# Optimization experiments

Hardware: AMD Instinct MI355X
Metric: run time of the kernel (lower is better)

## Reference

```python
import jax, jax.numpy as jnp
import numpy as np

B, C, H, W = 4, 256, 64, 64
N = H * W


def _conv1x1(x, w, b):
    # x: [B,C,H,W], w: [O,C], b: [O]  (1x1 conv == per-pixel linear)
    return jnp.einsum('bchw,oc->bohw', x, w) + b[None, :, None, None]


def setup_inputs() -> dict:
    key = jax.random.key(0)
    ks = jax.random.split(key, 11)
    s = 1.0 / np.sqrt(C)
    x = jax.random.normal(ks[0], (B, C, H, W), dtype=jnp.float32)
    mkw = lambda k: jax.random.normal(k, (C, C), dtype=jnp.float32) * s
    mkb = lambda k: jax.random.normal(k, (C,), dtype=jnp.float32) * 0.01
    return {
        'x': x,
        'w_teta': mkw(ks[1]), 'b_teta': mkb(ks[2]),
        'w_fi': mkw(ks[3]), 'b_fi': mkb(ks[4]),
        'w_gi': mkw(ks[5]), 'b_gi': mkb(ks[6]),
        'w_o1': mkw(ks[7]), 'b_o1': mkb(ks[8]),
        'w_o2': mkw(ks[9]), 'b_o2': mkb(ks[10]),
    }


def reference(x, w_teta, b_teta, w_fi, b_fi, w_gi, b_gi, w_o1, b_o1, w_o2, b_o2):
    b, c, h, w = x.shape
    n = h * w
    # 1x1 projections, flattened to [B,C,N]
    x1 = _conv1x1(x, w_teta, b_teta).reshape(b, c, n)
    x2 = _conv1x1(x, w_fi, b_fi).reshape(b, c, n)
    x3 = _conv1x1(x, w_gi, b_gi).reshape(b, c, n)
    # NOTE: original uses .view (memory reinterpretation), NOT transpose
    x1 = x1.reshape(b, n, c)
    x3 = x3.reshape(b, n, c)
    scores = jnp.einsum('bnc,bcm->bnm', x1, x2)      # [B,N,N]
    s_row = jax.nn.softmax(scores, axis=2)
    s_col = jax.nn.softmax(scores, axis=1)
    y1 = jnp.einsum('bnm,bmc->bnc', s_row, x3)       # [B,N,C]
    y2 = jnp.einsum('bnm,bmc->bnc', s_col, x3)
    # transpose(1,2) then view -> contiguous transpose + reshape
    y1 = jnp.swapaxes(y1, 1, 2).reshape(b, c, h, w)
    y2 = jnp.swapaxes(y2, 1, 2).reshape(b, c, h, w)
    o1 = _conv1x1(y1, w_o1, b_o1)
    o2 = _conv1x1(y2, w_o2, b_o2)
    xx = jnp.concatenate([x, x], axis=1)             # [B,2C,H,W]
    agg = jnp.concatenate([o1, o2], axis=1)
    return jax.nn.relu(xx + agg)
```

## Files before the change

kernel.cpp:

```cpp
#include <hip/hip_runtime.h>

#define BB   4
#define CC   256
#define NPIX 4096
#define AST2 40
#define YST  72

typedef __attribute__((ext_vector_type(8)))  short bf16x8;
typedef __attribute__((ext_vector_type(8)))  _Float16 f16x8;
typedef __attribute__((ext_vector_type(4)))  short short4v;
typedef __attribute__((ext_vector_type(16))) float f32x16;

__device__ __forceinline__ short f2h(float f) {
    _Float16 h = (_Float16)f;
    return __builtin_bit_cast(short, h);
}
__device__ __forceinline__ int cdrow(int r, int l5) {
    return (r & 3) + 8 * (r >> 2) + 4 * l5;
}
__device__ __forceinline__ short s_enc(float v) {
    float c = fmaxf(fminf(v, 127.9f), -127.9f);
    return (short)__float2int_rn(c * 256.0f);
}
__device__ __forceinline__ float s_dec(short v) {
    return (float)v * (1.0f / 256.0f);
}

__device__ __forceinline__ void mfma_core_f16(
    const short* __restrict__ A, const short* __restrict__ B, f32x16 acc[2][2])
{
    __shared__ short LA[128 * AST2], LB[128 * AST2];
    const int t = threadIdx.x;
    const int lane = t & 63, w = t >> 6;
    const int l31 = lane & 31, l5 = lane >> 5;
    const int nq = (w & 1) * 64, mq = (w >> 1) * 64;
    const int sr = t >> 1;
    const int sk = (t & 1) * 16;
    const size_t gs = (size_t)sr * 256 + sk;
    const int ls = sr * AST2 + sk;

    bf16x8 rA0 = *(const bf16x8*)(A + gs);
    bf16x8 rA1 = *(const bf16x8*)(A + gs + 8);
    bf16x8 rB0 = *(const bf16x8*)(B + gs);
    bf16x8 rB1 = *(const bf16x8*)(B + gs + 8);

    for (int k0 = 0; k0 < 256; k0 += 32) {
        __syncthreads();
        *(bf16x8*)&LA[ls]     = rA0;
        *(bf16x8*)&LA[ls + 8] = rA1;
        *(bf16x8*)&LB[ls]     = rB0;
        *(bf16x8*)&LB[ls + 8] = rB1;
        __syncthreads();
        if (k0 + 32 < 256) {
            size_t g = gs + k0 + 32;
            rA0 = *(const bf16x8*)(A + g);
            rA1 = *(const bf16x8*)(A + g + 8);
            rB0 = *(const bf16x8*)(B + g);
            rB1 = *(const bf16x8*)(B + g + 8);
        }
#pragma unroll
        for (int ks = 0; ks < 2; ks++) {
            f16x8 a[2], b[2];
#pragma unroll
            for (int s = 0; s < 2; s++) {
                a[s] = *(const f16x8*)&LA[(nq + s * 32 + l31) * AST2 + ks * 16 + l5 * 8];
                b[s] = *(const f16x8*)&LB[(mq + s * 32 + l31) * AST2 + ks * 16 + l5 * 8];
            }
#pragma unroll
            for (int s = 0; s < 2; s++)
#pragma unroll
                for (int u = 0; u < 2; u++)
                    acc[s][u] = __builtin_amdgcn_mfma_f32_32x32x16_f16(a[s], b[u], acc[s][u], 0, 0, 0);
        }
    }
}


__global__ __launch_bounds__(256) void pack_w5(
    const float* __restrict__ w0, const float* __restrict__ w1,
    const float* __restrict__ w2, const float* __restrict__ w3,
    const float* __restrict__ w4, short* __restrict__ wall)
{
    int which = blockIdx.y;
    const float* w = which == 0 ? w0 : which == 1 ? w1 : which == 2 ? w2
                   : which == 3 ? w3 : w4;
    int idx = blockIdx.x * 1024 + threadIdx.x * 4;
    float4 v = *(const float4*)(w + idx);
    short4v h;
    h.x = f2h(v.x); h.y = f2h(v.y); h.z = f2h(v.z); h.w = f2h(v.w);
    *(short4v*)(wall + which * 65536 + idx) = h;
}

__global__ __launch_bounds__(256) void pack_t_f16(
    const float* __restrict__ in, short* __restrict__ o16)
{
    __shared__ short T[32][36];
    const int b  = blockIdx.z;
    const int n0 = blockIdx.x * 32;
    const int c0 = blockIdx.y * 32;
    const float* src = in + (size_t)b * CC * NPIX;
    const int t = threadIdx.x;
    const int r = t >> 3, q = t & 7;
    float4 v = *(const float4*)(src + (size_t)(c0 + r) * NPIX + n0 + q * 4);
    T[q * 4 + 0][r] = f2h(v.x);
    T[q * 4 + 1][r] = f2h(v.y);
    T[q * 4 + 2][r] = f2h(v.z);
    T[q * 4 + 3][r] = f2h(v.w);
    __syncthreads();
    short4v o;
    o.x = T[r][q * 4 + 0];
    o.y = T[r][q * 4 + 1];
    o.z = T[r][q * 4 + 2];
    o.w = T[r][q * 4 + 3];
    size_t oo = (size_t)b * CC * NPIX + (size_t)(n0 + r) * 256 + c0 + q * 4;
    *(short4v*)(o16 + oo) = o;
}

__global__ __launch_bounds__(256) void tr16_cn(
    const short* __restrict__ in, short* __restrict__ outp)
{
    __shared__ short T[32][33];
    const int b  = blockIdx.z;
    const int n0 = blockIdx.x * 32;
    const int c0 = blockIdx.y * 32;
    const short* src = in + (size_t)b * CC * NPIX;
    short* dst = outp + (size_t)b * CC * NPIX;
    const int t = threadIdx.x;
    const int r = t >> 3, q = t & 7;
    short4v v = *(const short4v*)(src + (size_t)(c0 + r) * NPIX + n0 + q * 4);
    T[q * 4 + 0][r] = v.x;
    T[q * 4 + 1][r] = v.y;
    T[q * 4 + 2][r] = v.z;
    T[q * 4 + 3][r] = v.w;
    __syncthreads();
    short4v o;
    o.x = T[r][q * 4 + 0];
    o.y = T[r][q * 4 + 1];
    o.z = T[r][q * 4 + 2];
    o.w = T[r][q * 4 + 3];
    *(short4v*)(dst + (size_t)(n0 + r) * 256 + c0 + q * 4) = o;
}

__global__ __launch_bounds__(256) void packVt_bf(
    const short* __restrict__ x3f, short* __restrict__ Vt)
{
    __shared__ short T[32][33];
    const int b  = blockIdx.z;
    const int m0 = blockIdx.x * 32;
    const int c0 = blockIdx.y * 32;
    const short* in = x3f + (size_t)b * CC * NPIX;
    short* out = Vt + (size_t)b * CC * NPIX;
    const int t = threadIdx.x;
    const int r = t >> 3, q = t & 7;
    short4v v = *(const short4v*)(in + (size_t)(m0 + r) * CC + c0 + q * 4);
    T[q * 4 + 0][r] = v.x;
    T[q * 4 + 1][r] = v.y;
    T[q * 4 + 2][r] = v.z;
    T[q * 4 + 3][r] = v.w;
    __syncthreads();
    short4v o;
    o.x = T[r][q * 4 + 0];
    o.y = T[r][q * 4 + 1];
    o.z = T[r][q * 4 + 2];
    o.w = T[r][q * 4 + 3];
    *(short4v*)(out + (size_t)(c0 + r) * NPIX + m0 + q * 4) = o;
}


__global__ __launch_bounds__(256) void proj_mfma(
    const short* __restrict__ wpf, const short* __restrict__ xtf,
    const float* __restrict__ b_teta, const float* __restrict__ b_fi,
    const float* __restrict__ b_gi,
    short* __restrict__ x1f, short* __restrict__ x2f, short* __restrict__ x3f)
{
    const int z = blockIdx.z, p = z >> 2, b = z & 3;
    const int n0 = blockIdx.x * 128, c0 = blockIdx.y * 128;
    const size_t CN = (size_t)CC * NPIX;
    const short* Ah = wpf + p * 65536 + c0 * 256;
    const short* Bh = xtf + (size_t)b * CN + (size_t)n0 * 256;
    const float* bias = p == 0 ? b_teta : p == 1 ? b_fi : b_gi;
    short* dst = p == 0 ? x1f : p == 1 ? x2f : x3f;

    f32x16 acc[2][2] = {};
    mfma_core_f16(Ah, Bh, acc);

    const int t = threadIdx.x, lane = t & 63, w = t >> 6;
    const int l31 = lane & 31, l5 = lane >> 5;
    const int aq = (w & 1) * 64, bq = (w >> 1) * 64;
#pragma unroll
    for (int s = 0; s < 2; s++)
#pragma unroll
        for (int u = 0; u < 2; u++)
#pragma unroll
            for (int r = 0; r < 16; r++) {
                int c = c0 + aq + s * 32 + cdrow(r, l5);
                int n = n0 + bq + u * 32 + l31;
                float v = acc[s][u][r] + bias[c];
                size_t o = (size_t)b * CN + (size_t)c * NPIX + n;
                dst[o] = f2h(v);
            }
}

__global__ __launch_bounds__(256, 2) void scores_mfma(
    const short* __restrict__ x1f, const short* __restrict__ x2tf,
    short* __restrict__ S16, float* __restrict__ pm, float* __restrict__ pl)
{
    __shared__ short LA[256 * AST2];
    __shared__ short LB[128 * AST2];
    const int m0 = blockIdx.x * 128, n0 = blockIdx.y * 256;
    const short* A = x1f + (size_t)n0 * 256;
    const short* B = x2tf + (size_t)m0 * 256;

    const int t = threadIdx.x, lane = t & 63, w = t >> 6;
    const int l31 = lane & 31, l5 = lane >> 5;
    const int h = w & 1, g = w >> 1;

    const size_t gsA = (size_t)t * 256;
    const int lsA = t * AST2;
    const int srB = t >> 1, skB = (t & 1) * 16;
    const size_t gsB = (size_t)srB * 256 + skB;
    const int lsB = srB * AST2 + skB;

    bf16x8 rA0 = *(const bf16x8*)(A + gsA);
    bf16x8 rA1 = *(const bf16x8*)(A + gsA + 8);
    bf16x8 rA2 = *(const bf16x8*)(A + gsA + 16);
    bf16x8 rA3 = *(const bf16x8*)(A + gsA + 24);
    bf16x8 rB0 = *(const bf16x8*)(B + gsB);
    bf16x8 rB1 = *(const bf16x8*)(B + gsB + 8);

    f32x16 acc[4][2] = {};

    for (int k0 = 0; k0 < 256; k0 += 32) {
        __syncthreads();
        *(bf16x8*)&LA[lsA]      = rA0;
        *(bf16x8*)&LA[lsA + 8]  = rA1;
        *(bf16x8*)&LA[lsA + 16] = rA2;
        *(bf16x8*)&LA[lsA + 24] = rA3;
        *(bf16x8*)&LB[lsB]      = rB0;
        *(bf16x8*)&LB[lsB + 8]  = rB1;
        __syncthreads();
        if (k0 + 32 < 256) {
            size_t gA = gsA + k0 + 32;
            size_t gB = gsB + k0 + 32;
            rA0 = *(const bf16x8*)(A + gA);
            rA1 = *(const bf16x8*)(A + gA + 8);
            rA2 = *(const bf16x8*)(A + gA + 16);
            rA3 = *(const bf16x8*)(A + gA + 24);
            rB0 = *(const bf16x8*)(B + gB);
            rB1 = *(const bf16x8*)(B + gB + 8);
        }
#pragma unroll
        for (int ks = 0; ks < 2; ks++) {
            f16x8 a[4], b[2];
#pragma unroll
            for (int s = 0; s < 4; s++)
                a[s] = *(const f16x8*)&LA[(h * 128 + s * 32 + l31) * AST2 + ks * 16 + l5 * 8];
#pragma unroll
            for (int u = 0; u < 2; u++)
                b[u] = *(const f16x8*)&LB[(g * 64 + u * 32 + l31) * AST2 + ks * 16 + l5 * 8];
#pragma unroll
            for (int s = 0; s < 4; s++)
#pragma unroll
                for (int u = 0; u < 2; u++)
                    acc[s][u] = __builtin_amdgcn_mfma_f32_32x32x16_f16(a[s], b[u], acc[s][u], 0, 0, 0);
        }
    }

#pragma unroll
    for (int s = 0; s < 4; s++)
#pragma unroll
        for (int u = 0; u < 2; u++)
#pragma unroll
            for (int r = 0; r < 16; r++) {
                int n = n0 + h * 128 + s * 32 + cdrow(r, l5);
                int m = m0 + g * 64 + u * 32 + l31;
                S16[(size_t)n * NPIX + m] = s_enc(acc[s][u][r]);
            }

#pragma unroll
    for (int u = 0; u < 2; u++) {
        float vmax = -1e30f;
#pragma unroll
        for (int s = 0; s < 4; s++)
#pragma unroll
            for (int r = 0; r < 16; r++) vmax = fmaxf(vmax, acc[s][u][r]);
        float vsum = 0.0f;
#pragma unroll
        for (int s = 0; s < 4; s++)
#pragma unroll
            for (int r = 0; r < 16; r++) vsum += __expf(acc[s][u][r] - vmax);
        float vmax2 = __shfl_xor(vmax, 32, 64);
        float vsum2 = __shfl_xor(vsum, 32, 64);
        float mc = fmaxf(vmax, vmax2);
        float sc = vsum * __expf(vmax - mc) + vsum2 * __expf(vmax2 - mc);
        if (l5 == 0) {
            size_t pidx = (size_t)(blockIdx.y * 2 + h) * NPIX + m0 + g * 64 + u * 32 + l31;
            pm[pidx] = mc;
            pl[pidx] = sc;
        }
    }
}

__global__ __launch_bounds__(256) void out_mfma(
    const short* __restrict__ wof,
    const float* __restrict__ b_o1, const float* __restrict__ b_o2,
    const short* __restrict__ Yp,
    const float* __restrict__ x, float* __restrict__ out, int b)
{
    __shared__ short LA[128 * AST2], LB[128 * AST2];
    const size_t CN_ = (size_t)NPIX * CC;
    const int ch0 = blockIdx.y * 128;
    const int pix0 = blockIdx.x * 128;
    const int mode = ch0 < 256 ? 0 : 1;
    const short* W = wof + mode * 65536 + (size_t)(ch0 & 255) * 256;
    const short* Yq = Yp + (size_t)mode * 4 * CN_;
    const float* bias = mode == 0 ? b_o1 : b_o2;

    const int t = threadIdx.x, lane = t & 63, w = t >> 6;
    const int l31 = lane & 31, l5 = lane >> 5;
    const int nq = (w & 1) * 64, mq = (w >> 1) * 64;
    const int sr = t >> 1;
    const int sk = (t & 1) * 16;
    const size_t gsA = (size_t)sr * 256 + sk;
    const size_t gsB = (size_t)(pix0 + sr) * 256 + sk;
    const int ls = sr * AST2 + sk;

    f32x16 acc[2][2] = {};

    bf16x8 rA0 = *(const bf16x8*)(W + gsA);
    bf16x8 rA1 = *(const bf16x8*)(W + gsA + 8);
    f16x8 rB0, rB1;
    {
        rB0 = *(const f16x8*)(Yq + gsB);
        rB1 = *(const f16x8*)(Yq + gsB + 8);
#pragma unroll
        for (int q = 1; q < 4; q++) {
            rB0 = rB0 + *(const f16x8*)(Yq + (size_t)q * CN_ + gsB);
            rB1 = rB1 + *(const f16x8*)(Yq + (size_t)q * CN_ + gsB + 8);
        }
    }

    for (int k0 = 0; k0 < 256; k0 += 32) {
        __syncthreads();
        *(bf16x8*)&LA[ls]    = rA0;
        *(bf16x8*)&LA[ls + 8] = rA1;
        *(f16x8*)&LB[ls]     = rB0;
        *(f16x8*)&LB[ls + 8] = rB1;
        __syncthreads();
        if (k0 + 32 < 256) {
            size_t gA = gsA + k0 + 32;
            size_t gB = gsB + k0 + 32;
            rA0 = *(const bf16x8*)(W + gA);
            rA1 = *(const bf16x8*)(W + gA + 8);
            rB0 = *(const f16x8*)(Yq + gB);
            rB1 = *(const f16x8*)(Yq + gB + 8);
#pragma unroll
            for (int q = 1; q < 4; q++) {
                rB0 = rB0 + *(const f16x8*)(Yq + (size_t)q * CN_ + gB);
                rB1 = rB1 + *(const f16x8*)(Yq + (size_t)q * CN_ + gB + 8);
            }
        }
#pragma unroll
        for (int ks = 0; ks < 2; ks++) {
            f16x8 a[2], bb[2];
#pragma unroll
            for (int s = 0; s < 2; s++) {
                a[s]  = *(const f16x8*)&LA[(nq + s * 32 + l31) * AST2 + ks * 16 + l5 * 8];
                bb[s] = *(const f16x8*)&LB[(mq + s * 32 + l31) * AST2 + ks * 16 + l5 * 8];
            }
#pragma unroll
            for (int s = 0; s < 2; s++)
#pragma unroll
                for (int u = 0; u < 2; u++)
                    acc[s][u] = __builtin_amdgcn_mfma_f32_32x32x16_f16(a[s], bb[u], acc[s][u], 0, 0, 0);
        }
    }

    const int aq = (w & 1) * 64, bq = (w >> 1) * 64;
#pragma unroll
    for (int s = 0; s < 2; s++)
#pragma unroll
        for (int u = 0; u < 2; u++)
#pragma unroll
            for (int r = 0; r < 16; r++) {
                int ch = ch0 + aq + s * 32 + cdrow(r, l5);
                int pix = pix0 + bq + u * 32 + l31;
                int chm = ch & 255;
                float v = acc[s][u][r] + bias[chm] +
                          x[((size_t)b * CC + chm) * NPIX + pix];
                out[((size_t)b * 2 * CC + ch) * NPIX + pix] = fmaxf(v, 0.0f);
            }
}

__global__ __launch_bounds__(256) void stats16_kernel(
    const short* __restrict__ S16,
    const float* __restrict__ pm, const float* __restrict__ pl,
    float* __restrict__ cm, float* __restrict__ cli,
    float* __restrict__ rm, float* __restrict__ rli)
{
    __shared__ float sm[4][64], sl[4][64];
    __shared__ float red[4];
    const int t = threadIdx.x;
    if (blockIdx.x < 64) {
        const int cl = t & 63, ch = t >> 6;
        const int col = blockIdx.x * 64 + cl;
        float m = -1e30f, l = 0.0f;
        for (int i = ch * 8; i < ch * 8 + 8; i++) {
            float m2 = pm[(size_t)i * NPIX + col];
            float l2 = pl[(size_t)i * NPIX + col];
            float mn = fmaxf(m, m2);
            l = l * __expf(m - mn) + l2 * __expf(m2 - mn);
            m = mn;
        }
        sm[ch][cl] = m;
        sl[ch][cl] = l;
        __syncthreads();
        if (ch == 0) {
#pragma unroll
            for (int j = 1; j < 4; j++) {
                float m2 = sm[j][cl], l2 = sl[j][cl];
                float mn = fmaxf(m, m2);
                l = l * __expf(m - mn) + l2 * __expf(m2 - mn);
                m = mn;
            }
            cm[col]  = m;
            cli[col] = 1.0f / l;
        }
    } else {
        const int row = blockIdx.x - 64;
        const short* sp = S16 + (size_t)row * NPIX;
        const int w = t >> 6, lane = t & 63;
        float s4[16];
#pragma unroll
        for (int i = 0; i < 4; i++) {
            short4v v = *(const short4v*)(sp + (i * 256 + t) * 4);
            s4[i * 4 + 0] = s_dec(v.x);
            s4[i * 4 + 1] = s_dec(v.y);
            s4[i * 4 + 2] = s_dec(v.z);
            s4[i * 4 + 3] = s_dec(v.w);
        }
        float m = -1e30f;
#pragma unroll
        for (int i = 0; i < 16; i++) m = fmaxf(m, s4[i]);
        for (int off = 32; off; off >>= 1) m = fmaxf(m, __shfl_xor(m, off, 64));
        if (lane == 0) red[w] = m;
        __syncthreads();
        m = fmaxf(fmaxf(red[0], red[1]), fmaxf(red[2], red[3]));
        __syncthreads();
        float sum = 0.0f;
#pragma unroll
        for (int i = 0; i < 16; i++) sum += __expf(s4[i] - m);
        for (int off = 32; off; off >>= 1) sum += __shfl_xor(sum, off, 64);
        if (lane == 0) red[w] = sum;
        __syncthreads();
        if (t == 0) {
            rm[row]  = m;
            rli[row] = 1.0f / (red[0] + red[1] + red[2] + red[3]);
        }
    }
}

__device__ __forceinline__ void compute_ph(
    const short4v sv[4], int mode, int mg,
    const float* __restrict__ cmv, const float* __restrict__ cliv,
    float mrow, float lrow, short4v ph[4])
{
    if (mode == 0) {
#pragma unroll
        for (int i = 0; i < 4; i++) {
            ph[i].x = f2h(__expf(s_dec(sv[i].x) - mrow) * lrow);
            ph[i].y = f2h(__expf(s_dec(sv[i].y) - mrow) * lrow);
            ph[i].z = f2h(__expf(s_dec(sv[i].z) - mrow) * lrow);
            ph[i].w = f2h(__expf(s_dec(sv[i].w) - mrow) * lrow);
        }
    } else {
#pragma unroll
        for (int i = 0; i < 4; i++) {
            float4 cm4 = *(const float4*)(cmv + mg + i * 4);
            float4 cl4 = *(const float4*)(cliv + mg + i * 4);
            ph[i].x = f2h(__expf(s_dec(sv[i].x) - cm4.x) * cl4.x);
            ph[i].y = f2h(__expf(s_dec(sv[i].y) - cm4.y) * cl4.y);
            ph[i].z = f2h(__expf(s_dec(sv[i].z) - cm4.z) * cl4.z);
            ph[i].w = f2h(__expf(s_dec(sv[i].w) - cm4.w) * cl4.w);
        }
    }
}

__global__ __launch_bounds__(256) void pv_kernel(
    const short* __restrict__ S16, const short* __restrict__ Vt,
    const float* __restrict__ rmv, const float* __restrict__ rliv,
    const float* __restrict__ cmv, const float* __restrict__ cliv,
    short* __restrict__ Yp)
{
    __shared__ short LA[64 * YST];
    __shared__ short LB[256 * YST];
    const int mode = blockIdx.z, kq = blockIdx.y;
    const int n0 = blockIdx.x * 64;
    const int kbase = kq * 1024;

    const int t = threadIdx.x, lane = t & 63, w = t >> 6;
    const int l31 = lane & 31, l5 = lane >> 5;
    const int nst = (w & 1) * 32, cb = (w >> 1) * 128;
    const int ar = t >> 2;
    const int ak = (t & 3) * 16;

    const float mrow = rmv[n0 + ar];
    const float lrow = rliv[n0 + ar];
    const short* sp = S16 + (size_t)(n0 + ar) * NPIX + kbase + ak;

    short4v svA[4], svB[4];
    bf16x8 pbA[8], pbB[8];
#pragma unroll
    for (int i = 0; i < 4; i++) {
        svA[i] = *(const short4v*)(sp + i * 4);
        svB[i] = *(const short4v*)(sp + 64 + i * 4);
    }
#pragma unroll
    for (int i = 0; i < 4; i++) {
        const short* bp0 = Vt + (size_t)(i * 64 + ar) * NPIX + kbase + ak;
        pbA[2 * i]     = *(const bf16x8*)bp0;
        pbA[2 * i + 1] = *(const bf16x8*)(bp0 + 8);
        pbB[2 * i]     = *(const bf16x8*)(bp0 + 64);
        pbB[2 * i + 1] = *(const bf16x8*)(bp0 + 72);
    }

    f32x16 acc[4] = {};
    for (int sx = 0; sx < 8; sx++) {
        const int s = sx * 2;
        {
            short4v ph[4];
            compute_ph(svA, mode, kbase + s * 64 + ak, cmv, cliv, mrow, lrow, ph);
            __syncthreads();
#pragma unroll
            for (int i = 0; i < 4; i++)
                *(short4v*)&LA[ar * YST + ak + i * 4] = ph[i];
#pragma unroll
            for (int i = 0; i < 4; i++) {
                *(bf16x8*)&LB[(i * 64 + ar) * YST + ak]     = pbA[2 * i];
                *(bf16x8*)&LB[(i * 64 + ar) * YST + ak + 8] = pbA[2 * i + 1];
            }
            __syncthreads();
            if (s + 2 < 16) {
                const short* spn = sp + (s + 2) * 64;
#pragma unroll
                for (int i = 0; i < 4; i++)
                    svA[i] = *(const short4v*)(spn + i * 4);
                int kg = kbase + (s + 2) * 64 + ak;
#pragma unroll
                for (int i = 0; i < 4; i++) {
                    const short* bp = Vt + (size_t)(i * 64 + ar) * NPIX + kg;
                    pbA[2 * i]     = *(const bf16x8*)bp;
                    pbA[2 * i + 1] = *(const bf16x8*)(bp + 8);
                }
            }
#pragma unroll
            for (int kc = 0; kc < 4; kc++) {
                f16x8 af = *(const f16x8*)&LA[(nst + l31) * YST + kc * 16 + l5 * 8];
#pragma unroll
                for (int u = 0; u < 4; u++) {
                    f16x8 bf = *(const f16x8*)&LB[(cb + u * 32 + l31) * YST + kc * 16 + l5 * 8];
                    acc[u] = __builtin_amdgcn_mfma_f32_32x32x16_f16(af, bf, acc[u], 0, 0, 0);
                }
            }
        }
        {
            short4v ph[4];
            compute_ph(svB, mode, kbase + (s + 1) * 64 + ak, cmv, cliv, mrow, lrow, ph);
            __syncthreads();
#pragma unroll
            for (int i = 0; i < 4; i++)
                *(short4v*)&LA[ar * YST + ak + i * 4] = ph[i];
#pragma unroll
            for (int i = 0; i < 4; i++) {
                *(bf16x8*)&LB[(i * 64 + ar) * YST + ak]     = pbB[2 * i];
                *(bf16x8*)&LB[(i * 64 + ar) * YST + ak + 8] = pbB[2 * i + 1];
            }
            __syncthreads();
            if (s + 3 < 16) {
                const short* spn = sp + (s + 3) * 64;
#pragma unroll
                for (int i = 0; i < 4; i++)
                    svB[i] = *(const short4v*)(spn + i * 4);
                int kg = kbase + (s + 3) * 64 + ak;
#pragma unroll
                for (int i = 0; i < 4; i++) {
                    const short* bp = Vt + (size_t)(i * 64 + ar) * NPIX + kg;
                    pbB[2 * i]     = *(const bf16x8*)bp;
                    pbB[2 * i + 1] = *(const bf16x8*)(bp + 8);
                }
            }
#pragma unroll
            for (int kc = 0; kc < 4; kc++) {
                f16x8 af = *(const f16x8*)&LA[(nst + l31) * YST + kc * 16 + l5 * 8];
#pragma unroll
                for (int u = 0; u < 4; u++) {
                    f16x8 bf = *(const f16x8*)&LB[(cb + u * 32 + l31) * YST + kc * 16 + l5 * 8];
                    acc[u] = __builtin_amdgcn_mfma_f32_32x32x16_f16(af, bf, acc[u], 0, 0, 0);
                }
            }
        }
    }

    short* Yo = Yp + (size_t)(mode * 4 + kq) * ((size_t)NPIX * CC);
#pragma unroll
    for (int u = 0; u < 4; u++)
#pragma unroll
        for (int r = 0; r < 16; r++) {
            int rr = cdrow(r, l5);
            Yo[(size_t)(n0 + nst + rr) * CC + cb + u * 32 + l31] = f2h(acc[u][r]);
        }
}

extern "C" void kernel_launch(void* const* d_in, const int* in_sizes, int n_in,
                              void* d_out, int out_size, void* d_ws, size_t ws_size,
                              hipStream_t stream)
{
    (void)in_sizes; (void)n_in; (void)out_size; (void)ws_size;
    const float* x      = (const float*)d_in[0];
    const float* w_teta = (const float*)d_in[1];
    const float* b_teta = (const float*)d_in[2];
    const float* w_fi   = (const float*)d_in[3];
    const float* b_fi   = (const float*)d_in[4];
    const float* w_gi   = (const float*)d_in[5];
    const float* b_gi   = (const float*)d_in[6];
    const float* w_o1   = (const float*)d_in[7];
    const float* b_o1   = (const float*)d_in[8];
    const float* w_o2   = (const float*)d_in[9];
    const float* b_o2   = (const float*)d_in[10];
    float* out = (float*)d_out;

    const size_t CN = (size_t)CC * NPIX;
    const size_t NN = (size_t)NPIX * NPIX;
    short* wsp   = (short*)d_ws;
    short* S16   = wsp;
    short* Yp    = S16 + NN;
    short* x1f   = Yp + 16 * CN;
    short* x2tf  = x1f + BB * CN;
    short* Vtb   = x2tf + BB * CN;
    float* cm    = (float*)(Vtb + BB * CN);
    float* cli   = cm + NPIX;
    float* rm    = cli + NPIX;
    float* rli   = rm + NPIX;
    float* pm    = rli + NPIX;
    float* pl    = pm + 64 * NPIX;
    short* wall  = (short*)(pl + 64 * NPIX);
    short* wpf   = wall;
    short* wof   = wall + 3 * 65536;
    short* xtf  = Yp;
    short* x2f  = S16;
    short* x3f  = S16 + BB * CN;

    dim3 blk(256);
    pack_w5<<<dim3(64, 5), blk, 0, stream>>>(w_teta, w_fi, w_gi, w_o1, w_o2, wall);
    pack_t_f16<<<dim3(128, 8, 4), blk, 0, stream>>>(x, xtf);

    proj_mfma<<<dim3(32, 2, 12), blk, 0, stream>>>(
        wpf, xtf, b_teta, b_fi, b_gi, x1f, x2f, x3f);

    tr16_cn<<<dim3(128, 8, 4), blk, 0, stream>>>(x2f, x2tf);
    packVt_bf<<<dim3(128, 8, 4), blk, 0, stream>>>(x3f, Vtb);

    for (int b = 0; b < BB; b++) {
        scores_mfma<<<dim3(32, 16), blk, 0, stream>>>(
            x1f + b * CN, x2tf + b * CN, S16, pm, pl);
        stats16_kernel<<<dim3(64 + NPIX), blk, 0, stream>>>(
            S16, pm, pl, cm, cli, rm, rli);
        pv_kernel<<<dim3(64, 4, 2), blk, 0, stream>>>(
            S16, Vtb + b * CN, rm, rli, cm, cli, Yp);
        out_mfma<<<dim3(32, 4), blk, 0, stream>>>(
            wof, b_o1, b_o2, Yp, x, out, b);
    }
}
```

Measured before the change: 448.9 us.

## Enlarge PV tile to 128 rows and split K into eight partial sums

The PV kernel now computes 128 query rows per block instead of 64, with each wave doing a 2x4 MFMA tile. The block covers 512 keys instead of 1024, so the K dimension is split into eight partial outputs. This raises reuse of the V tile staged in shared memory and simplifies the single-buffered loop. In exchange the output projection kernel must read and sum eight partial Y buffers instead of four, and the partial workspace doubles.

```diff
diff --git a/kernel.cpp b/kernel.cpp
--- a/kernel.cpp
+++ b/kernel.cpp
@@ -313,7 +313,7 @@
     const int pix0 = blockIdx.x * 128;
     const int mode = ch0 < 256 ? 0 : 1;
     const short* W = wof + mode * 65536 + (size_t)(ch0 & 255) * 256;
-    const short* Yq = Yp + (size_t)mode * 4 * CN_;
+    const short* Yq = Yp + (size_t)mode * 8 * CN_;
     const float* bias = mode == 0 ? b_o1 : b_o2;
 
     const int t = threadIdx.x, lane = t & 63, w = t >> 6;
@@ -334,7 +334,7 @@
         rB0 = *(const f16x8*)(Yq + gsB);
         rB1 = *(const f16x8*)(Yq + gsB + 8);
 #pragma unroll
-        for (int q = 1; q < 4; q++) {
+        for (int q = 1; q < 8; q++) {
             rB0 = rB0 + *(const f16x8*)(Yq + (size_t)q * CN_ + gsB);
             rB1 = rB1 + *(const f16x8*)(Yq + (size_t)q * CN_ + gsB + 8);
         }
@@ -355,7 +355,7 @@
             rB0 = *(const f16x8*)(Yq + gB);
             rB1 = *(const f16x8*)(Yq + gB + 8);
 #pragma unroll
-            for (int q = 1; q < 4; q++) {
+            for (int q = 1; q < 8; q++) {
                 rB0 = rB0 + *(const f16x8*)(Yq + (size_t)q * CN_ + gB);
                 rB1 = rB1 + *(const f16x8*)(Yq + (size_t)q * CN_ + gB + 8);
             }
@@ -460,155 +460,127 @@
     }
 }
 
-__device__ __forceinline__ void compute_ph(
-    const short4v sv[4], int mode, int mg,
-    const float* __restrict__ cmv, const float* __restrict__ cliv,
-    float mrow, float lrow, short4v ph[4])
-{
-    if (mode == 0) {
-#pragma unroll
-        for (int i = 0; i < 4; i++) {
-            ph[i].x = f2h(__expf(s_dec(sv[i].x) - mrow) * lrow);
-            ph[i].y = f2h(__expf(s_dec(sv[i].y) - mrow) * lrow);
-            ph[i].z = f2h(__expf(s_dec(sv[i].z) - mrow) * lrow);
-            ph[i].w = f2h(__expf(s_dec(sv[i].w) - mrow) * lrow);
-        }
-    } else {
-#pragma unroll
-        for (int i = 0; i < 4; i++) {
-            float4 cm4 = *(const float4*)(cmv + mg + i * 4);
-            float4 cl4 = *(const float4*)(cliv + mg + i * 4);
-            ph[i].x = f2h(__expf(s_dec(sv[i].x) - cm4.x) * cl4.x);
-            ph[i].y = f2h(__expf(s_dec(sv[i].y) - cm4.y) * cl4.y);
-            ph[i].z = f2h(__expf(s_dec(sv[i].z) - cm4.z) * cl4.z);
-            ph[i].w = f2h(__expf(s_dec(sv[i].w) - cm4.w) * cl4.w);
-        }
-    }
-}
-
 __global__ __launch_bounds__(256) void pv_kernel(
     const short* __restrict__ S16, const short* __restrict__ Vt,
     const float* __restrict__ rmv, const float* __restrict__ rliv,
     const float* __restrict__ cmv, const float* __restrict__ cliv,
     short* __restrict__ Yp)
 {
-    __shared__ short LA[64 * YST];
+    __shared__ short LA[128 * YST];
     __shared__ short LB[256 * YST];
     const int mode = blockIdx.z, kq = blockIdx.y;
-    const int n0 = blockIdx.x * 64;
-    const int kbase = kq * 1024;
+    const int n0 = blockIdx.x * 128;
+    const int kbase = kq * 512;
 
     const int t = threadIdx.x, lane = t & 63, w = t >> 6;
     const int l31 = lane & 31, l5 = lane >> 5;
-    const int nst = (w & 1) * 32, cb = (w >> 1) * 128;
-    const int ar = t >> 2;
-    const int ak = (t & 3) * 16;
+    const int nst = (w & 1) * 64, cb = (w >> 1) * 128;
+    const int ar = t >> 1;
+    const int ak = (t & 1) * 32;
+    const int br = t >> 1;
+    const int bk = (t & 1) * 32;
 
     const float mrow = rmv[n0 + ar];
     const float lrow = rliv[n0 + ar];
-    const short* sp = S16 + (size_t)(n0 + ar) * NPIX + kbase + ak;
-
-    short4v svA[4], svB[4];
-    bf16x8 pbA[8], pbB[8];
-#pragma unroll
-    for (int i = 0; i < 4; i++) {
-        svA[i] = *(const short4v*)(sp + i * 4);
-        svB[i] = *(const short4v*)(sp + 64 + i * 4);
-    }
-#pragma unroll
-    for (int i = 0; i < 4; i++) {
-        const short* bp0 = Vt + (size_t)(i * 64 + ar) * NPIX + kbase + ak;
-        pbA[2 * i]     = *(const bf16x8*)bp0;
-        pbA[2 * i + 1] = *(const bf16x8*)(bp0 + 8);
-        pbB[2 * i]     = *(const bf16x8*)(bp0 + 64);
-        pbB[2 * i + 1] = *(const bf16x8*)(bp0 + 72);
-    }
-
-    f32x16 acc[4] = {};
-    for (int sx = 0; sx < 8; sx++) {
-        const int s = sx * 2;
-        {
-            short4v ph[4];
-            compute_ph(svA, mode, kbase + s * 64 + ak, cmv, cliv, mrow, lrow, ph);
-            __syncthreads();
-#pragma unroll
-            for (int i = 0; i < 4; i++)
-                *(short4v*)&LA[ar * YST + ak + i * 4] = ph[i];
-#pragma unroll
-            for (int i = 0; i < 4; i++) {
-                *(bf16x8*)&LB[(i * 64 + ar) * YST + ak]     = pbA[2 * i];
-                *(bf16x8*)&LB[(i * 64 + ar) * YST + ak + 8] = pbA[2 * i + 1];
-            }
-            __syncthreads();
-            if (s + 2 < 16) {
-                const short* spn = sp + (s + 2) * 64;
-#pragma unroll
-                for (int i = 0; i < 4; i++)
-                    svA[i] = *(const short4v*)(spn + i * 4);
-                int kg = kbase + (s + 2) * 64 + ak;
-#pragma unroll
-                for (int i = 0; i < 4; i++) {
-                    const short* bp = Vt + (size_t)(i * 64 + ar) * NPIX + kg;
-                    pbA[2 * i]     = *(const bf16x8*)bp;
-                    pbA[2 * i + 1] = *(const bf16x8*)(bp + 8);
-                }
-            }
-#pragma unroll
-            for (int kc = 0; kc < 4; kc++) {
-                f16x8 af = *(const f16x8*)&LA[(nst + l31) * YST + kc * 16 + l5 * 8];
-#pragma unroll
-                for (int u = 0; u < 4; u++) {
-                    f16x8 bf = *(const f16x8*)&LB[(cb + u * 32 + l31) * YST + kc * 16 + l5 * 8];
-                    acc[u] = __builtin_amdgcn_mfma_f32_32x32x16_f16(af, bf, acc[u], 0, 0, 0);
-                }
-            }
-        }
-        {
-            short4v ph[4];
-            compute_ph(svB, mode, kbase + (s + 1) * 64 + ak, cmv, cliv, mrow, lrow, ph);
-            __syncthreads();
-#pragma unroll
-            for (int i = 0; i < 4; i++)
-                *(short4v*)&LA[ar * YST + ak + i * 4] = ph[i];
-#pragma unroll
-            for (int i = 0; i < 4; i++) {
-                *(bf16x8*)&LB[(i * 64 + ar) * YST + ak]     = pbB[2 * i];
-                *(bf16x8*)&LB[(i * 64 + ar) * YST + ak + 8] = pbB[2 * i + 1];
-            }
-            __syncthreads();
-            if (s + 3 < 16) {
-                const short* spn = sp + (s + 3) * 64;
-#pragma unroll
-                for (int i = 0; i < 4; i++)
-                    svB[i] = *(const short4v*)(spn + i * 4);
-                int kg = kbase + (s + 3) * 64 + ak;
-#pragma unroll
-                for (int i = 0; i < 4; i++) {
-                    const short* bp = Vt + (size_t)(i * 64 + ar) * NPIX + kg;
-                    pbB[2 * i]     = *(const bf16x8*)bp;
-                    pbB[2 * i + 1] = *(const bf16x8*)(bp + 8);
-                }
-            }
-#pragma unroll
-            for (int kc = 0; kc < 4; kc++) {
-                f16x8 af = *(const f16x8*)&LA[(nst + l31) * YST + kc * 16 + l5 * 8];
-#pragma unroll
-                for (int u = 0; u < 4; u++) {
-                    f16x8 bf = *(const f16x8*)&LB[(cb + u * 32 + l31) * YST + kc * 16 + l5 * 8];
-                    acc[u] = __builtin_amdgcn_mfma_f32_32x32x16_f16(af, bf, acc[u], 0, 0, 0);
-                }
-            }
-        }
-    }
-
-    short* Yo = Yp + (size_t)(mode * 4 + kq) * ((size_t)NPIX * CC);
-#pragma unroll
-    for (int u = 0; u < 4; u++)
-#pragma unroll
-        for (int r = 0; r < 16; r++) {
-            int rr = cdrow(r, l5);
-            Yo[(size_t)(n0 + nst + rr) * CC + cb + u * 32 + l31] = f2h(acc[u][r]);
-        }
+    const short* sp  = S16 + (size_t)(n0 + ar) * NPIX + kbase + ak;
+    const short* vp0 = Vt + (size_t)br * NPIX + kbase + bk;
+    const short* vp1 = vp0 + (size_t)128 * NPIX;
+
+    short4v sv[8];
+    bf16x8 pb0[2], pb1[2];
+#pragma unroll
+    for (int i = 0; i < 8; i++)
+        sv[i] = *(const short4v*)(sp + i * 4);
+#pragma unroll
+    for (int j = 0; j < 2; j++) {
+        pb0[j] = *(const bf16x8*)(vp0 + j * 16);
+        pb1[j] = *(const bf16x8*)(vp1 + j * 16);
+    }
+    bf16x8 pb0b[2], pb1b[2];
+    pb0b[0] = *(const bf16x8*)(vp0 + 8);
+    pb0b[1] = *(const bf16x8*)(vp0 + 24);
+    pb1b[0] = *(const bf16x8*)(vp1 + 8);
+    pb1b[1] = *(const bf16x8*)(vp1 + 24);
+
+    f32x16 acc[2][4] = {};
+    for (int s = 0; s < 8; s++) {
+        short4v ph[8];
+        if (mode == 0) {
+#pragma unroll
+            for (int i = 0; i < 8; i++) {
+                ph[i].x = f2h(__expf(s_dec(sv[i].x) - mrow) * lrow);
+                ph[i].y = f2h(__expf(s_dec(sv[i].y) - mrow) * lrow);
+                ph[i].z = f2h(__expf(s_dec(sv[i].z) - mrow) * lrow);
+                ph[i].w = f2h(__expf(s_dec(sv[i].w) - mrow) * lrow);
+            }
+        } else {
+            const int mg = kbase + s * 64 + ak;
+#pragma unroll
+            for (int i = 0; i < 8; i++) {
+                float4 cm4 = *(const float4*)(cmv + mg + i * 4);
+                float4 cl4 = *(const float4*)(cliv + mg + i * 4);
+                ph[i].x = f2h(__expf(s_dec(sv[i].x) - cm4.x) * cl4.x);
+                ph[i].y = f2h(__expf(s_dec(sv[i].y) - cm4.y) * cl4.y);
+                ph[i].z = f2h(__expf(s_dec(sv[i].z) - cm4.z) * cl4.z);
+                ph[i].w = f2h(__expf(s_dec(sv[i].w) - cm4.w) * cl4.w);
+            }
+        }
+        __syncthreads();
+#pragma unroll
+        for (int i = 0; i < 8; i++)
+            *(short4v*)&LA[ar * YST + ak + i * 4] = ph[i];
+        *(bf16x8*)&LB[br * YST + bk]            = pb0[0];
+        *(bf16x8*)&LB[br * YST + bk + 8]        = pb0b[0];
+        *(bf16x8*)&LB[br * YST + bk + 16]       = pb0[1];
+        *(bf16x8*)&LB[br * YST + bk + 24]       = pb0b[1];
+        *(bf16x8*)&LB[(br + 128) * YST + bk]      = pb1[0];
+        *(bf16x8*)&LB[(br + 128) * YST + bk + 8]  = pb1b[0];
+        *(bf16x8*)&LB[(br + 128) * YST + bk + 16] = pb1[1];
+        *(bf16x8*)&LB[(br + 128) * YST + bk + 24] = pb1b[1];
+        __syncthreads();
+        if (s + 1 < 8) {
+            const short* spn = sp + (s + 1) * 64;
+#pragma unroll
+            for (int i = 0; i < 8; i++)
+                sv[i] = *(const short4v*)(spn + i * 4);
+            const short* vn0 = vp0 + (s + 1) * 64;
+            const short* vn1 = vp1 + (s + 1) * 64;
+            pb0[0]  = *(const bf16x8*)(vn0);
+            pb0b[0] = *(const bf16x8*)(vn0 + 8);
+            pb0[1]  = *(const bf16x8*)(vn0 + 16);
+            pb0b[1] = *(const bf16x8*)(vn0 + 24);
+            pb1[0]  = *(const bf16x8*)(vn1);
+            pb1b[0] = *(const bf16x8*)(vn1 + 8);
+            pb1[1]  = *(const bf16x8*)(vn1 + 16);
+            pb1b[1] = *(const bf16x8*)(vn1 + 24);
+        }
+#pragma unroll
+        for (int kc = 0; kc < 4; kc++) {
+            f16x8 af[2], bf[4];
+#pragma unroll
+            for (int si = 0; si < 2; si++)
+                af[si] = *(const f16x8*)&LA[(nst + si * 32 + l31) * YST + kc * 16 + l5 * 8];
+#pragma unroll
+            for (int u = 0; u < 4; u++)
+                bf[u] = *(const f16x8*)&LB[(cb + u * 32 + l31) * YST + kc * 16 + l5 * 8];
+#pragma unroll
+            for (int si = 0; si < 2; si++)
+#pragma unroll
+                for (int u = 0; u < 4; u++)
+                    acc[si][u] = __builtin_amdgcn_mfma_f32_32x32x16_f16(af[si], bf[u], acc[si][u], 0, 0, 0);
+        }
+    }
+
+    short* Yo = Yp + (size_t)(mode * 8 + kq) * ((size_t)NPIX * CC);
+#pragma unroll
+    for (int si = 0; si < 2; si++)
+#pragma unroll
+        for (int u = 0; u < 4; u++)
+#pragma unroll
+            for (int r = 0; r < 16; r++) {
+                int rr = cdrow(r, l5);
+                Yo[(size_t)(n0 + nst + si * 32 + rr) * CC + cb + u * 32 + l31] = f2h(acc[si][u][r]);
+            }
 }
 
 extern "C" void kernel_launch(void* const* d_in, const int* in_sizes, int n_in,
@@ -665,7 +637,7 @@
             x1f + b * CN, x2tf + b * CN, S16, pm, pl);
         stats16_kernel<<<dim3(64 + NPIX), blk, 0, stream>>>(
             S16, pm, pl, cm, cli, rm, rli);
-        pv_kernel<<<dim3(64, 4, 2), blk, 0, stream>>>(
+        pv_kernel<<<dim3(32, 8, 2), blk, 0, stream>>>(
             S16, Vtb + b * CN, rm, rli, cm, cli, Yp);
         out_mfma<<<dim3(32, 4), blk, 0, stream>>>(
             wof, b_o1, b_o2, Yp, x, out, b);
```

Result: slower. 475.8 us (+6.0%).
